# Kernel optimization log

Measured on AMD Instinct MI355X. Metric: run time of the kernel, lower is better.

The kernel has to match this reference:

```python
import jax, jax.numpy as jnp
import numpy as np

K_NEIGHBORS = 16
IGNORE_INDEX = -1
LOSS_WEIGHT = 1.0
N_POINTS = 262144
NUM_CLASSES = 20


def setup_inputs() -> dict:
    key = jax.random.key(0)
    k1, k2, k3, k4 = jax.random.split(key, 4)
    seg_logits = jax.random.normal(k1, (N_POINTS, NUM_CLASSES), dtype=jnp.float32)
    coord = jax.random.normal(k2, (N_POINTS, 3), dtype=jnp.float32)
    labels = jax.random.randint(k3, (N_POINTS,), 0, NUM_CLASSES, dtype=jnp.int64)
    # KNN indices are computed under no_grad in the original (pointops.knn_query);
    # here they are synthetic in-range indices (no -1 padding entries).
    reference_index = jax.random.randint(k4, (N_POINTS, K_NEIGHBORS), 0, N_POINTS, dtype=jnp.int64)
    return {
        "seg_logits": seg_logits,
        "coord": coord,
        "labels": labels,
        "reference_index": reference_index,
    }


def reference(seg_logits, coord, labels, reference_index):
    # coord is only used by the (no-grad) KNN query in the original; indices are given.
    probs = jax.nn.softmax(seg_logits, axis=1)              # [N, C]
    idx = jnp.maximum(reference_index, 0)                   # safe gather index
    knn_mask = reference_index >= 0                         # sign(idx+1).bool()
    neighbor_labels = labels[idx]                           # [N, k]
    same_label_mask = labels[:, None] == neighbor_labels
    center_valid = (labels != IGNORE_INDEX)[:, None]
    neighbor_valid = neighbor_labels != IGNORE_INDEX
    total_mask = knn_mask & center_valid & neighbor_valid & same_label_mask  # [N, k]

    neighbor_probs = probs[idx]                             # [N, k, C]
    prob_dist_sq = jnp.sum((probs[:, None, :] - neighbor_probs) ** 2, axis=2)  # [N, k]
    sum_loss = jnp.sum(prob_dist_sq * total_mask.astype(probs.dtype))
    num_valid = jnp.maximum(jnp.sum(total_mask).astype(probs.dtype), 1.0)
    return (sum_loss / num_valid) * LOSS_WEIGHT
```

## Files before the change

kernel.cpp:

```cpp
#include <hip/hip_runtime.h>

#define NCLS 20
#define IGNORE_INDEX (-1)
#define TPB 128
#define PAIRS_PER_THREAD 8
#define PPB (TPB * PAIRS_PER_THREAD)
#define BLOCKS 4096
#define RBITS 18

__device__ __forceinline__ void softmax_row(const float* __restrict__ row, float* v) {
    const float4* r4 = (const float4*)row;
#pragma unroll
    for (int q = 0; q < 5; ++q) {
        float4 t = r4[q];
        v[4 * q + 0] = t.x; v[4 * q + 1] = t.y;
        v[4 * q + 2] = t.z; v[4 * q + 3] = t.w;
    }
    float mx = v[0];
#pragma unroll
    for (int c = 1; c < NCLS; ++c) mx = fmaxf(mx, v[c]);
    float s = 0.f;
#pragma unroll
    for (int c = 0; c < NCLS; ++c) { v[c] = __expf(v[c] - mx); s += v[c]; }
    float inv = 1.0f / s;
#pragma unroll
    for (int c = 0; c < NCLS; ++c) v[c] *= inv;
}

__global__ __launch_bounds__(TPB) void fused_kernel(
    const float* __restrict__ logits, const int* __restrict__ labels,
    const int* __restrict__ ref_idx,
    unsigned int* __restrict__ counts, float* __restrict__ partials,
    long long total_pairs) {
    __shared__ unsigned int s_buf[PPB];
    __shared__ int s_cnt;
    __shared__ float s_wsum[TPB / 64];
    const int tid = threadIdx.x;
    if (tid == 0) s_cnt = 0;
    __syncthreads();

    const long long pair0 = (long long)blockIdx.x * PPB + (long long)tid * 8;
    if (pair0 + 8 <= total_pairs) {
        const int p = (int)(pair0 >> 4);
        const int li = labels[p];
        int4 ra = *(const int4*)(ref_idx + pair0);
        int4 rb = *(const int4*)(ref_idx + pair0 + 4);
        int rr[8] = {ra.x, ra.y, ra.z, ra.w, rb.x, rb.y, rb.z, rb.w};
        int nl[8];
#pragma unroll
        for (int j = 0; j < 8; ++j) nl[j] = labels[max(rr[j], 0)];
        if (li != IGNORE_INDEX) {
#pragma unroll
            for (int j = 0; j < 8; ++j) {
                if (rr[j] >= 0 && nl[j] == li) {
                    int slot = atomicAdd(&s_cnt, 1);
                    s_buf[slot] = ((unsigned int)(tid * 8 + j) << RBITS) |
                                  (unsigned int)rr[j];
                }
            }
        }
    }
    __syncthreads();
    const int c = s_cnt;

    float fsum = 0.f;
    for (int i = tid; i < c; i += TPB) {
        unsigned int e = s_buf[i];
        unsigned int lid = e >> RBITS;
        unsigned int r = e & ((1u << RBITS) - 1u);
        unsigned int p = (unsigned int)blockIdx.x * (PPB / 16) + (lid >> 4);
        float a[NCLS], b[NCLS];
        softmax_row(logits + (size_t)p * NCLS, a);
        softmax_row(logits + (size_t)r * NCLS, b);
        float d = 0.f;
#pragma unroll
        for (int k = 0; k < NCLS; ++k) {
            float dx = a[k] - b[k];
            d = fmaf(dx, dx, d);
        }
        fsum += d;
    }

#pragma unroll
    for (int off = 32; off > 0; off >>= 1) fsum += __shfl_down(fsum, off, 64);
    if ((tid & 63) == 0) s_wsum[tid >> 6] = fsum;
    __syncthreads();
    if (tid == 0) {
        float t = 0.f;
#pragma unroll
        for (int w = 0; w < TPB / 64; ++w) t += s_wsum[w];
        partials[blockIdx.x] = t;
        counts[blockIdx.x] = (unsigned int)c;
    }
}

__global__ __launch_bounds__(1024) void reduce_kernel(
    const float* __restrict__ partials, const unsigned int* __restrict__ counts,
    float* __restrict__ out, int m) {
    double dsum = 0.0;
    unsigned long long cnt = 0;
    for (int i = threadIdx.x; i < m; i += 1024) {
        dsum += (double)partials[i];
        cnt  += (unsigned long long)min(counts[i], (unsigned int)PPB);
    }
#pragma unroll
    for (int off = 32; off > 0; off >>= 1) {
        dsum += __shfl_down(dsum, off, 64);
        cnt  += __shfl_down(cnt,  off, 64);
    }
    __shared__ double s_sum[16];
    __shared__ unsigned long long s_cnt[16];
    const int wave = threadIdx.x >> 6;
    if ((threadIdx.x & 63) == 0) { s_sum[wave] = dsum; s_cnt[wave] = cnt; }
    __syncthreads();
    if (threadIdx.x == 0) {
        double ts = 0.0; unsigned long long tc = 0;
        for (int w = 0; w < 16; ++w) { ts += s_sum[w]; tc += s_cnt[w]; }
        if (tc < 1ull) tc = 1ull;
        out[0] = (float)(ts / (double)tc);
    }
}

extern "C" void kernel_launch(void* const* d_in, const int* in_sizes, int n_in,
                              void* d_out, int out_size, void* d_ws, size_t ws_size,
                              hipStream_t stream) {
    const float* seg_logits = (const float*)d_in[0];
    const int* labels  = (const int*)d_in[2];
    const int* ref_idx = (const int*)d_in[3];
    float* out = (float*)d_out;
    const int n = in_sizes[2];
    const long long total_pairs = (long long)n * 16;

    unsigned int* counts = (unsigned int*)d_ws;
    float* partials      = (float*)((char*)d_ws + BLOCKS * 4);

    fused_kernel<<<BLOCKS, TPB, 0, stream>>>(seg_logits, labels, ref_idx,
                                             counts, partials, total_pairs);
    reduce_kernel<<<1, 1024, 0, stream>>>(partials, counts, out, BLOCKS);
}
```

Before: 102.0 us.

## Prefilter neighbor labels with shared-memory 2-bit label hash table

Adds a prep kernel that packs the low two bits of every label into a 64 KB bitfield. Each block loads the whole table into LDS so most neighbor-label mismatches are rejected without a random global gather; only hash hits read the real label. The shared-memory compaction buffer is dropped, and matching pairs are computed inline per thread at 1024 threads per block. The large LDS footprint limits occupancy, and inline work per thread causes wave divergence.

After: 123.4 us. 1.21x slower.

```diff
diff --git a/kernel.cpp b/kernel.cpp
--- a/kernel.cpp
+++ b/kernel.cpp
@@ -2,11 +2,10 @@
 
 #define NCLS 20
 #define IGNORE_INDEX (-1)
-#define TPB 128
+#define TPB 1024
 #define PAIRS_PER_THREAD 8
 #define PPB (TPB * PAIRS_PER_THREAD)
-#define BLOCKS 4096
-#define RBITS 18
+#define HASH_WORDS 16384
 
 __device__ __forceinline__ void softmax_row(const float* __restrict__ row, float* v) {
     const float4* r4 = (const float4*)row;
@@ -27,70 +26,94 @@
     for (int c = 0; c < NCLS; ++c) v[c] *= inv;
 }
 
+__global__ __launch_bounds__(256) void hash_prep(const int* __restrict__ labels,
+                                                 unsigned int* __restrict__ H,
+                                                 int words) {
+    int w = blockIdx.x * blockDim.x + threadIdx.x;
+    if (w >= words) return;
+    const int4* lp = (const int4*)(labels + (size_t)w * 16);
+    int4 v0 = lp[0], v1 = lp[1], v2 = lp[2], v3 = lp[3];
+    int l[16] = {v0.x, v0.y, v0.z, v0.w, v1.x, v1.y, v1.z, v1.w,
+                 v2.x, v2.y, v2.z, v2.w, v3.x, v3.y, v3.z, v3.w};
+    unsigned int acc = 0;
+#pragma unroll
+    for (int k = 0; k < 16; ++k)
+        acc |= ((unsigned int)(l[k] & 3)) << (2 * k);
+    H[w] = acc;
+}
+
 __global__ __launch_bounds__(TPB) void fused_kernel(
     const float* __restrict__ logits, const int* __restrict__ labels,
-    const int* __restrict__ ref_idx,
+    const int* __restrict__ ref_idx, const unsigned int* __restrict__ H,
     unsigned int* __restrict__ counts, float* __restrict__ partials,
     long long total_pairs) {
-    __shared__ unsigned int s_buf[PPB];
-    __shared__ int s_cnt;
-    __shared__ float s_wsum[TPB / 64];
+    __shared__ unsigned int s_hash[HASH_WORDS];
     const int tid = threadIdx.x;
-    if (tid == 0) s_cnt = 0;
+
+    {
+        const uint4* src = (const uint4*)H;
+        uint4* dst = (uint4*)s_hash;
+#pragma unroll
+        for (int i = 0; i < 4; ++i) dst[tid + i * TPB] = src[tid + i * TPB];
+    }
     __syncthreads();
 
-    const long long pair0 = (long long)blockIdx.x * PPB + (long long)tid * 8;
-    if (pair0 + 8 <= total_pairs) {
+    float fsum = 0.f;
+    unsigned int cnt = 0;
+    const long long pair0 = (long long)blockIdx.x * PPB +
+                            (long long)tid * PAIRS_PER_THREAD;
+    if (pair0 + PAIRS_PER_THREAD <= total_pairs) {
         const int p = (int)(pair0 >> 4);
         const int li = labels[p];
         int4 ra = *(const int4*)(ref_idx + pair0);
         int4 rb = *(const int4*)(ref_idx + pair0 + 4);
         int rr[8] = {ra.x, ra.y, ra.z, ra.w, rb.x, rb.y, rb.z, rb.w};
-        int nl[8];
-#pragma unroll
-        for (int j = 0; j < 8; ++j) nl[j] = labels[max(rr[j], 0)];
         if (li != IGNORE_INDEX) {
+            const unsigned int h_li = (unsigned int)(li & 3);
+            unsigned int hv[8];
 #pragma unroll
             for (int j = 0; j < 8; ++j) {
-                if (rr[j] >= 0 && nl[j] == li) {
-                    int slot = atomicAdd(&s_cnt, 1);
-                    s_buf[slot] = ((unsigned int)(tid * 8 + j) << RBITS) |
-                                  (unsigned int)rr[j];
+                int idx = max(rr[j], 0);
+                hv[j] = (s_hash[idx >> 4] >> (2 * (idx & 15))) & 3u;
+            }
+#pragma unroll
+            for (int j = 0; j < 8; ++j) {
+                if (rr[j] >= 0 && hv[j] == h_li) {
+                    int nl = labels[rr[j]];
+                    if (nl == li) {
+                        float a[NCLS], b[NCLS];
+                        softmax_row(logits + (size_t)p * NCLS, a);
+                        softmax_row(logits + (size_t)rr[j] * NCLS, b);
+                        float d = 0.f;
+#pragma unroll
+                        for (int k = 0; k < NCLS; ++k) {
+                            float dx = a[k] - b[k];
+                            d = fmaf(dx, dx, d);
+                        }
+                        fsum += d;
+                        cnt += 1u;
+                    }
                 }
             }
         }
     }
-    __syncthreads();
-    const int c = s_cnt;
-
-    float fsum = 0.f;
-    for (int i = tid; i < c; i += TPB) {
-        unsigned int e = s_buf[i];
-        unsigned int lid = e >> RBITS;
-        unsigned int r = e & ((1u << RBITS) - 1u);
-        unsigned int p = (unsigned int)blockIdx.x * (PPB / 16) + (lid >> 4);
-        float a[NCLS], b[NCLS];
-        softmax_row(logits + (size_t)p * NCLS, a);
-        softmax_row(logits + (size_t)r * NCLS, b);
-        float d = 0.f;
-#pragma unroll
-        for (int k = 0; k < NCLS; ++k) {
-            float dx = a[k] - b[k];
-            d = fmaf(dx, dx, d);
-        }
-        fsum += d;
-    }
 
 #pragma unroll
-    for (int off = 32; off > 0; off >>= 1) fsum += __shfl_down(fsum, off, 64);
-    if ((tid & 63) == 0) s_wsum[tid >> 6] = fsum;
+    for (int off = 32; off > 0; off >>= 1) {
+        fsum += __shfl_down(fsum, off, 64);
+        cnt  += __shfl_down(cnt,  off, 64);
+    }
+    __syncthreads();
+    float* s_f        = (float*)s_hash;
+    unsigned int* s_c = s_hash + 64;
+    if ((tid & 63) == 0) { s_f[tid >> 6] = fsum; s_c[tid >> 6] = cnt; }
     __syncthreads();
     if (tid == 0) {
-        float t = 0.f;
+        float ts = 0.f; unsigned int tc = 0;
 #pragma unroll
-        for (int w = 0; w < TPB / 64; ++w) t += s_wsum[w];
-        partials[blockIdx.x] = t;
-        counts[blockIdx.x] = (unsigned int)c;
+        for (int w = 0; w < TPB / 64; ++w) { ts += s_f[w]; tc += s_c[w]; }
+        partials[blockIdx.x] = ts;
+        counts[blockIdx.x] = tc;
     }
 }
 
@@ -130,11 +153,14 @@
     float* out = (float*)d_out;
     const int n = in_sizes[2];
     const long long total_pairs = (long long)n * 16;
+    const int blocks = (int)((total_pairs + PPB - 1) / PPB);
 
-    unsigned int* counts = (unsigned int*)d_ws;
-    float* partials      = (float*)((char*)d_ws + BLOCKS * 4);
+    unsigned int* H        = (unsigned int*)d_ws;
+    unsigned int* counts   = (unsigned int*)((char*)d_ws + HASH_WORDS * 4);
+    float* partials        = (float*)((char*)d_ws + HASH_WORDS * 4 + 512 * 4);
 
-    fused_kernel<<<BLOCKS, TPB, 0, stream>>>(seg_logits, labels, ref_idx,
+    hash_prep<<<(HASH_WORDS + 255) / 256, 256, 0, stream>>>(labels, H, HASH_WORDS);
+    fused_kernel<<<blocks, TPB, 0, stream>>>(seg_logits, labels, ref_idx, H,
                                              counts, partials, total_pairs);
-    reduce_kernel<<<1, 1024, 0, stream>>>(partials, counts, out, BLOCKS);
+    reduce_kernel<<<1, 1024, 0, stream>>>(partials, counts, out, blocks);
 }
```
